# Performance work log

Measured on AMD Instinct MI355X. Metric: run time of the kernel, lower is better.

## Reference

```python
import jax, jax.numpy as jnp
import numpy as np

ALPHA_U = 1.0 / 10.0   # dt/tauu
ALPHA_V = 1.0 / 150.0  # dt/tauv
M = 10.0

def setup_inputs() -> dict:
    key = jax.random.key(0)
    ks = jax.random.split(key, 6)
    B, D_in, H = 8192, 1024, 2048
    stdv = 1.0 / np.sqrt(H)
    return {
        "x": jax.random.normal(ks[0], (B, D_in), dtype=jnp.float32),
        "u": jax.random.normal(ks[1], (B, H), dtype=jnp.float32),
        "v": jax.random.normal(ks[2], (B, H), dtype=jnp.float32),
        "win": jax.random.uniform(ks[3], (H, D_in), dtype=jnp.float32, minval=-stdv, maxval=stdv),
        "wr": jax.random.uniform(ks[4], (H, H), dtype=jnp.float32, minval=-stdv, maxval=stdv),
        "bias": jax.random.uniform(ks[5], (H,), dtype=jnp.float32, minval=-stdv, maxval=stdv),
    }

def reference(x, u, v, win, wr, bias):
    # v update: leaky blend toward m*u, then relu
    v_new = jax.nn.relu((1.0 - ALPHA_V) * v + (ALPHA_V * M) * u)
    # u update: leaky blend with input + recurrent drive minus adapted v
    drive = jnp.einsum('bi,hi->bh', x, win) + jnp.einsum('bk,hk->bh', u, wr) + bias - v_new
    u_new = jax.nn.relu((1.0 - ALPHA_U) * u + ALPHA_U * drive)
    return (u_new, v_new)
```

## Files before the change

kernel.cpp:

```cpp
#include <hip/hip_runtime.h>
#include <hip/hip_bf16.h>
#include <stdint.h>

#define B_DIM 8192
#define D_IN  1024
#define H_DIM 2048
#define K_DIM (D_IN + H_DIM)

#define ALPHA_U (1.0f/10.0f)
#define ALPHA_V (1.0f/150.0f)
#define M_CONST 10.0f

typedef __attribute__((ext_vector_type(8))) short short8;
typedef __attribute__((ext_vector_type(4))) float floatx4;

__device__ __forceinline__ unsigned short f2bf(float f) {
    union { float f; unsigned u; } x; x.f = f;
    unsigned r = x.u + 0x7fffu + ((x.u >> 16) & 1u);
    return (unsigned short)(r >> 16);
}

__global__ void pack_bf16(const float4* __restrict__ src, unsigned short* __restrict__ dst,
                          int shift, int mask, int col_off, int total4) {
    int i = blockIdx.x * blockDim.x + threadIdx.x;
    if (i >= total4) return;
    int idx = i << 2;
    int r = idx >> shift;
    int c = idx & mask;
    float4 f = src[i];
    ushort4 o;
    o.x = f2bf(f.x); o.y = f2bf(f.y); o.z = f2bf(f.z); o.w = f2bf(f.w);
    *(ushort4*)(dst + (size_t)r * K_DIM + col_off + c) = o;
}

#define GLOAD_LDS16(gp, lp)                                                          \
    __builtin_amdgcn_global_load_lds(                                                \
        (const __attribute__((address_space(1))) unsigned int*)(gp),                 \
        (__attribute__((address_space(3))) unsigned int*)(lp), 16, 0, 0)

__global__ __launch_bounds__(256)
void gemm_fused(const unsigned short* __restrict__ A,
                const unsigned short* __restrict__ Wc,
                const float* __restrict__ u_in,
                const float* __restrict__ v_in,
                const float* __restrict__ bias,
                float* __restrict__ out)
{
    __shared__ __align__(16) unsigned short As[128 * 32];
    __shared__ __align__(16) unsigned short Bs[128 * 32];

    const int tid  = threadIdx.x;
    const int wave = tid >> 6;
    const int lane = tid & 63;
    const int bm = blockIdx.y;
    const int bn = blockIdx.x;

    const int srow = lane >> 2;
    const int scol = (lane & 3) * 8;
    const unsigned short* Ag = A  + (size_t)(bm * 128 + wave * 32 + srow) * K_DIM + scol;
    const unsigned short* Bg = Wc + (size_t)(bn * 128 + wave * 32 + srow) * K_DIM + scol;
    unsigned short* AsW = As + wave * 1024;
    unsigned short* BsW = Bs + wave * 1024;

    const int wm = (wave >> 1) * 64;
    const int wn = (wave & 1) * 64;
    const int frow = lane & 15;
    const int fk   = (lane >> 4) * 8;

    floatx4 acc[4][4] = {};

    for (int k0 = 0; k0 < K_DIM; k0 += 32) {
        GLOAD_LDS16(Ag + k0,              AsW);
        GLOAD_LDS16(Ag + 16 * K_DIM + k0, AsW + 512);
        GLOAD_LDS16(Bg + k0,              BsW);
        GLOAD_LDS16(Bg + 16 * K_DIM + k0, BsW + 512);
        __syncthreads();

        short8 af[4], bfr[4];
#pragma unroll
        for (int i = 0; i < 4; i++)
            af[i] = *(const short8*)&As[(wm + i * 16 + frow) * 32 + fk];
#pragma unroll
        for (int j = 0; j < 4; j++)
            bfr[j] = *(const short8*)&Bs[(wn + j * 16 + frow) * 32 + fk];

#pragma unroll
        for (int i = 0; i < 4; i++)
#pragma unroll
            for (int j = 0; j < 4; j++)
                acc[i][j] = __builtin_amdgcn_mfma_f32_16x16x32_bf16(
                    af[i], bfr[j], acc[i][j], 0, 0, 0);
        __syncthreads();
    }

    const size_t outV = (size_t)B_DIM * H_DIM;
    const int rbase = (lane >> 4) * 4;
    const int cbase = lane & 15;
#pragma unroll
    for (int i = 0; i < 4; i++) {
#pragma unroll
        for (int j = 0; j < 4; j++) {
            const int col = bn * 128 + wn + j * 16 + cbase;
            const float bcol = bias[col];
#pragma unroll
            for (int r = 0; r < 4; r++) {
                const int row = bm * 128 + wm + i * 16 + rbase + r;
                const size_t idx = (size_t)row * H_DIM + col;
                const float uu = u_in[idx];
                const float vv = v_in[idx];
                const float vn = fmaxf((1.0f - ALPHA_V) * vv + (ALPHA_V * M_CONST) * uu, 0.0f);
                const float drive = acc[i][j][r] + bcol - vn;
                const float un = fmaxf((1.0f - ALPHA_U) * uu + ALPHA_U * drive, 0.0f);
                out[idx] = un;
                out[outV + idx] = vn;
            }
        }
    }
}

extern "C" void kernel_launch(void* const* d_in, const int* in_sizes, int n_in,
                              void* d_out, int out_size, void* d_ws, size_t ws_size,
                              hipStream_t stream) {
    const float* x    = (const float*)d_in[0];
    const float* u    = (const float*)d_in[1];
    const float* v    = (const float*)d_in[2];
    const float* win  = (const float*)d_in[3];
    const float* wr   = (const float*)d_in[4];
    const float* bias = (const float*)d_in[5];
    float* out = (float*)d_out;

    unsigned short* Abf = (unsigned short*)d_ws;
    unsigned short* Wbf = Abf + (size_t)B_DIM * K_DIM;

    const int threads = 256;
    {
        int total4 = (B_DIM * D_IN) / 4;
        pack_bf16<<<total4 / threads, threads, 0, stream>>>(
            (const float4*)x, Abf, 10, 1023, 0, total4);
    }
    {
        int total4 = (B_DIM * H_DIM) / 4;
        pack_bf16<<<total4 / threads, threads, 0, stream>>>(
            (const float4*)u, Abf, 11, 2047, D_IN, total4);
    }
    {
        int total4 = (H_DIM * D_IN) / 4;
        pack_bf16<<<total4 / threads, threads, 0, stream>>>(
            (const float4*)win, Wbf, 10, 1023, 0, total4);
    }
    {
        int total4 = (H_DIM * H_DIM) / 4;
        pack_bf16<<<total4 / threads, threads, 0, stream>>>(
            (const float4*)wr, Wbf, 11, 2047, D_IN, total4);
    }

    dim3 grid(H_DIM / 128, B_DIM / 128);
    gemm_fused<<<grid, 256, 0, stream>>>(Abf, Wbf, u, v, bias, out);
}
```

Baseline: 443.2 us.

## Swizzle LDS tiles, remap blocks, vectorize epilogue via LDS, merge pack kernels

Four bf16 pack launches are merged into one kernel. The GEMM stages tiles in LDS with an XOR-style column swizzle to cut bank conflicts on fragment reads, and remaps block IDs (grouped by 8) for better L2 reuse. The epilogue goes through LDS so it can use float4 loads and stores of u, v and the outputs instead of scalar strided accesses, and launch bounds request 4 blocks per CU. The main risks are extra LDS traffic in the epilogue and a possible register limit from the occupancy hint.

```diff
diff --git a/kernel.cpp b/kernel.cpp
--- a/kernel.cpp
+++ b/kernel.cpp
@@ -7,9 +7,10 @@
 #define H_DIM 2048
 #define K_DIM (D_IN + H_DIM)
 
-#define ALPHA_U (1.0f/10.0f)
-#define ALPHA_V (1.0f/150.0f)
-#define M_CONST 10.0f
+#define CV_CONST  (1.0f - 1.0f/150.0f)
+#define CUV_CONST (10.0f/150.0f)
+#define CU_CONST  0.9f
+#define AU_CONST  0.1f
 
 typedef __attribute__((ext_vector_type(8))) short short8;
 typedef __attribute__((ext_vector_type(4))) float floatx4;
@@ -20,17 +21,29 @@
     return (unsigned short)(r >> 16);
 }
 
-__global__ void pack_bf16(const float4* __restrict__ src, unsigned short* __restrict__ dst,
-                          int shift, int mask, int col_off, int total4) {
-    int i = blockIdx.x * blockDim.x + threadIdx.x;
-    if (i >= total4) return;
+#define N4_X   ((B_DIM * D_IN)  / 4)
+#define N4_U   ((B_DIM * H_DIM) / 4)
+#define N4_WIN ((H_DIM * D_IN)  / 4)
+#define N4_WR  ((H_DIM * H_DIM) / 4)
+#define N4_TOT (N4_X + N4_U + N4_WIN + N4_WR)
+
+__global__ __launch_bounds__(256)
+void pack_all(const float4* __restrict__ x, const float4* __restrict__ u,
+              const float4* __restrict__ win, const float4* __restrict__ wr,
+              unsigned short* __restrict__ Abf, unsigned short* __restrict__ Wbf) {
+    int i = blockIdx.x * 256 + threadIdx.x;
+    const float4* src; unsigned short* dst; int shift, mask, coloff;
+    if (i < N4_X)                    { src = x;   dst = Abf; shift = 10; mask = 1023; coloff = 0;    }
+    else if (i < N4_X + N4_U)        { i -= N4_X; src = u;   dst = Abf; shift = 11; mask = 2047; coloff = D_IN; }
+    else if (i < N4_X + N4_U + N4_WIN){ i -= N4_X + N4_U; src = win; dst = Wbf; shift = 10; mask = 1023; coloff = 0; }
+    else                             { i -= N4_X + N4_U + N4_WIN; src = wr; dst = Wbf; shift = 11; mask = 2047; coloff = D_IN; }
     int idx = i << 2;
     int r = idx >> shift;
     int c = idx & mask;
     float4 f = src[i];
     ushort4 o;
     o.x = f2bf(f.x); o.y = f2bf(f.y); o.z = f2bf(f.z); o.w = f2bf(f.w);
-    *(ushort4*)(dst + (size_t)r * K_DIM + col_off + c) = o;
+    *(ushort4*)(dst + (size_t)r * K_DIM + coloff + c) = o;
 }
 
 #define GLOAD_LDS16(gp, lp)                                                          \
@@ -38,7 +51,11 @@
         (const __attribute__((address_space(1))) unsigned int*)(gp),                 \
         (__attribute__((address_space(3))) unsigned int*)(lp), 16, 0, 0)
 
-__global__ __launch_bounds__(256)
+#define ES_STRIDE 68
+#define ES_REGION (16 * ES_STRIDE)
+#define SMEM_BYTES (8 * ES_REGION * 4)
+
+__global__ __launch_bounds__(256, 4)
 void gemm_fused(const unsigned short* __restrict__ A,
                 const unsigned short* __restrict__ Wc,
                 const float* __restrict__ u_in,
@@ -46,17 +63,23 @@
                 const float* __restrict__ bias,
                 float* __restrict__ out)
 {
-    __shared__ __align__(16) unsigned short As[128 * 32];
-    __shared__ __align__(16) unsigned short Bs[128 * 32];
+    __shared__ __align__(16) unsigned char smem_raw[SMEM_BYTES];
+    unsigned short* As = (unsigned short*)smem_raw;
+    unsigned short* Bs = As + 128 * 32;
+    float* Esf = (float*)smem_raw;
 
     const int tid  = threadIdx.x;
     const int wave = tid >> 6;
     const int lane = tid & 63;
-    const int bm = blockIdx.y;
-    const int bn = blockIdx.x;
+
+    const int bid = blockIdx.x;
+    const int wid = ((bid & 7) << 7) | (bid >> 3);
+    const int bm = wid >> 4;
+    const int bn = wid & 15;
 
     const int srow = lane >> 2;
-    const int scol = (lane & 3) * 8;
+    const int gcar = ((lane & 3) - ((lane >> 3) & 3)) & 3;
+    const int scol = gcar * 8;
     const unsigned short* Ag = A  + (size_t)(bm * 128 + wave * 32 + srow) * K_DIM + scol;
     const unsigned short* Bg = Wc + (size_t)(bn * 128 + wave * 32 + srow) * K_DIM + scol;
     unsigned short* AsW = As + wave * 1024;
@@ -65,7 +88,8 @@
     const int wm = (wave >> 1) * 64;
     const int wn = (wave & 1) * 64;
     const int frow = lane & 15;
-    const int fk   = (lane >> 4) * 8;
+    const int g    = lane >> 4;
+    const int swz  = ((g + (frow >> 1)) & 3) * 8;
 
     floatx4 acc[4][4] = {};
 
@@ -79,10 +103,10 @@
         short8 af[4], bfr[4];
 #pragma unroll
         for (int i = 0; i < 4; i++)
-            af[i] = *(const short8*)&As[(wm + i * 16 + frow) * 32 + fk];
+            af[i] = *(const short8*)&As[(wm + i * 16 + frow) * 32 + swz];
 #pragma unroll
         for (int j = 0; j < 4; j++)
-            bfr[j] = *(const short8*)&Bs[(wn + j * 16 + frow) * 32 + fk];
+            bfr[j] = *(const short8*)&Bs[(wn + j * 16 + frow) * 32 + swz];
 
 #pragma unroll
         for (int i = 0; i < 4; i++)
@@ -93,27 +117,39 @@
         __syncthreads();
     }
 
+    const int q   = lane >> 4;
+    const int c16 = lane & 15;
+    const int rbase = q * 4;
+    const int colg = bn * 128 + wn + c16 * 4;
+    const float4 b4 = *(const float4*)&bias[colg];
     const size_t outV = (size_t)B_DIM * H_DIM;
-    const int rbase = (lane >> 4) * 4;
-    const int cbase = lane & 15;
+
 #pragma unroll
     for (int i = 0; i < 4; i++) {
+        float* Es = Esf + (wave * 2 + (i & 1)) * ES_REGION;
 #pragma unroll
-        for (int j = 0; j < 4; j++) {
-            const int col = bn * 128 + wn + j * 16 + cbase;
-            const float bcol = bias[col];
+        for (int j = 0; j < 4; j++)
 #pragma unroll
-            for (int r = 0; r < 4; r++) {
-                const int row = bm * 128 + wm + i * 16 + rbase + r;
-                const size_t idx = (size_t)row * H_DIM + col;
-                const float uu = u_in[idx];
-                const float vv = v_in[idx];
-                const float vn = fmaxf((1.0f - ALPHA_V) * vv + (ALPHA_V * M_CONST) * uu, 0.0f);
-                const float drive = acc[i][j][r] + bcol - vn;
-                const float un = fmaxf((1.0f - ALPHA_U) * uu + ALPHA_U * drive, 0.0f);
-                out[idx] = un;
-                out[outV + idx] = vn;
-            }
+            for (int r = 0; r < 4; r++)
+                Es[(rbase + r) * ES_STRIDE + j * 16 + c16] = acc[i][j][r];
+#pragma unroll
+        for (int rg = 0; rg < 4; rg++) {
+            const int rloc = rg * 4 + q;
+            const float4 a4 = *(const float4*)&Es[rloc * ES_STRIDE + c16 * 4];
+            const size_t idx = (size_t)(bm * 128 + wm + i * 16 + rloc) * H_DIM + colg;
+            const float4 u4 = *(const float4*)&u_in[idx];
+            const float4 v4 = *(const float4*)&v_in[idx];
+            float4 vn, un;
+            vn.x = fmaxf(CV_CONST * v4.x + CUV_CONST * u4.x, 0.0f);
+            vn.y = fmaxf(CV_CONST * v4.y + CUV_CONST * u4.y, 0.0f);
+            vn.z = fmaxf(CV_CONST * v4.z + CUV_CONST * u4.z, 0.0f);
+            vn.w = fmaxf(CV_CONST * v4.w + CUV_CONST * u4.w, 0.0f);
+            un.x = fmaxf(CU_CONST * u4.x + AU_CONST * (a4.x + b4.x - vn.x), 0.0f);
+            un.y = fmaxf(CU_CONST * u4.y + AU_CONST * (a4.y + b4.y - vn.y), 0.0f);
+            un.z = fmaxf(CU_CONST * u4.z + AU_CONST * (a4.z + b4.z - vn.z), 0.0f);
+            un.w = fmaxf(CU_CONST * u4.w + AU_CONST * (a4.w + b4.w - vn.w), 0.0f);
+            *(float4*)&out[idx]        = un;
+            *(float4*)&out[outV + idx] = vn;
         }
     }
 }
@@ -132,28 +168,9 @@
     unsigned short* Abf = (unsigned short*)d_ws;
     unsigned short* Wbf = Abf + (size_t)B_DIM * K_DIM;
 
-    const int threads = 256;
-    {
-        int total4 = (B_DIM * D_IN) / 4;
-        pack_bf16<<<total4 / threads, threads, 0, stream>>>(
-            (const float4*)x, Abf, 10, 1023, 0, total4);
-    }
-    {
-        int total4 = (B_DIM * H_DIM) / 4;
-        pack_bf16<<<total4 / threads, threads, 0, stream>>>(
-            (const float4*)u, Abf, 11, 2047, D_IN, total4);
-    }
-    {
-        int total4 = (H_DIM * D_IN) / 4;
-        pack_bf16<<<total4 / threads, threads, 0, stream>>>(
-            (const float4*)win, Wbf, 10, 1023, 0, total4);
-    }
-    {
-        int total4 = (H_DIM * H_DIM) / 4;
-        pack_bf16<<<total4 / threads, threads, 0, stream>>>(
-            (const float4*)wr, Wbf, 11, 2047, D_IN, total4);
-    }
+    pack_all<<<N4_TOT / 256, 256, 0, stream>>>(
+        (const float4*)x, (const float4*)u, (const float4*)win, (const float4*)wr,
+        Abf, Wbf);
 
-    dim3 grid(H_DIM / 128, B_DIM / 128);
-    gemm_fused<<<grid, 256, 0, stream>>>(Abf, Wbf, u, v, bias, out);
+    gemm_fused<<<1024, 256, 0, stream>>>(Abf, Wbf, u, v, bias, out);
 }
```

After: 401.5 us. 1.1x faster.
